# Kernel tuning notes

Measured on AMD Instinct MI355X. Metric: run time of the kernel, lower is better.

The kernel has to match this reference:

```python
import jax, jax.numpy as jnp
import numpy as np

SAMPLE_RATE = 16000
SOUND_SPEED = 343.0
MAX_ORDER = 15
RIR_LENGTH = 3968
WINDOW_LENGTH = 81
PAD = WINDOW_LENGTH // 2  # 40

# Static image-source lattice (depends only on max_order): all integer
# reflection index triplets with |nx|+|ny|+|nz| <= max_order.
_ind = np.arange(-MAX_ORDER, MAX_ORDER + 1)
_grid = np.stack(np.meshgrid(_ind, _ind, _ind, indexing="ij"), -1).reshape(-1, 3)
XYZ = _grid[np.abs(_grid).sum(1) <= MAX_ORDER].astype(np.float32)  # (I,3), I=4991
EXP_LO = np.abs(np.floor(XYZ / 2)).astype(np.float32)        # hits on lower walls per dim
EXP_HI = np.abs(np.floor((XYZ + 1) / 2)).astype(np.float32)  # hits on upper walls per dim


def _hann(x, T):
    # continuous Hann window sampled at non-integer points, zero outside |x|<=T/2
    return jnp.where(jnp.abs(x) <= T / 2, 0.5 * (1.0 + jnp.cos(2.0 * jnp.pi * x / T)), 0.0)


def _forward(inp):
    room = inp[:, 0:3]                 # (B,3) room dimensions [m]
    mic = inp[:, 3:6] * room           # (B,3)
    src = inp[:, 6:9] * room           # (B,3)
    a_w = inp[:, 9:10]
    absorption = jnp.concatenate([a_w, a_w, a_w, a_w, inp[:, 10:11], inp[:, 11:12]], axis=1)
    absorption = absorption * 0.84 + 0.01            # (B,6): [x-,x+,y-,y+,floor,ceiling]
    tr = jnp.sqrt(1.0 - absorption)                  # wall reflection coefficients

    xyz = jnp.asarray(XYZ)                           # (I,3)
    d = room[:, None, :]
    s = src[:, None, :]
    # image source locations (B,I,3): mirror parity per torchaudio ISM
    img_loc = jnp.where(xyz % 2 == 1, d * (xyz + 1.0) - s, d * xyz + s)
    # per-image-source attenuation (B,I)
    t_lo = tr[:, None, 0::2]                         # (B,1,3) lower walls per dim
    t_hi = tr[:, None, 1::2]                         # (B,1,3) upper walls per dim
    att = jnp.prod(t_lo ** jnp.asarray(EXP_LO) * t_hi ** jnp.asarray(EXP_HI), axis=-1)

    dist = jnp.linalg.norm(img_loc - mic[:, None, :], axis=-1)   # (B,I)
    amp = att / dist                                              # 1/r spreading
    delay = dist * (SAMPLE_RATE / SOUND_SPEED)                    # fractional sample delay
    delay_i = jnp.ceil(delay)

    # windowed-sinc fractional-delay pulse sampled at n = delay_i-PAD .. delay_i+PAD
    n_rel = jnp.arange(-PAD, PAD + 1, dtype=jnp.float32)          # (W,)
    x = delay_i[..., None] + n_rel - delay[..., None]             # (B,I,W)
    sig = amp[..., None] * jnp.sinc(x) * _hann(x, 2 * PAD)        # (B,I,W)

    # scatter-accumulate pulses at time index n, dropping out-of-range samples
    t_idx = (delay_i[..., None] + n_rel).astype(jnp.int32)        # (B,I,W)
    B = inp.shape[0]
    b_idx = jnp.arange(B, dtype=jnp.int32)[:, None, None]
    rir = jnp.zeros((B, RIR_LENGTH), dtype=sig.dtype).at[b_idx, t_idx].add(sig, mode="drop")

    toa = PAD + SAMPLE_RATE * jnp.linalg.norm(mic - src, axis=1) / SOUND_SPEED  # (B,)
    return rir, toa


def setup_inputs():
    key = jax.random.key(0)
    u = jax.random.uniform(key, (128, 12), dtype=jnp.float32)
    room = 2.0 + 8.0 * u[:, :3]          # room dims in [2,10] m
    rest = 0.05 + 0.9 * u[:, 3:]         # mic/src fractions and absorptions in (0,1)
    return {"input": jnp.concatenate([room, rest], axis=1)}


def reference(input):
    return _forward(input)
```

## Files before the change

kernel.cpp:

```cpp
#include <hip/hip_runtime.h>

#define NIMG    4991
#define RIRLEN  3968
#define NT      512
#define NW      31
#define KPT     10
#define INV_PI  0.31830988618379067f
#define SR_OVER_C 46.647230320699704f

struct Tab { int v[NIMG]; };
static constexpr Tab make_tab() {
    Tab t{};
    int k = 0;
    for (int x = -15; x <= 15; ++x)
        for (int y = -15; y <= 15; ++y)
            for (int z = -15; z <= 15; ++z) {
                int ax = x < 0 ? -x : x;
                int ay = y < 0 ? -y : y;
                int az = z < 0 ? -z : z;
                if (ax + ay + az <= 15)
                    t.v[k++] = (x + 15) | ((y + 15) << 8) | ((z + 15) << 16);
            }
    return t;
}
__constant__ Tab c_tab = make_tab();

static __device__ __forceinline__ int iabs(int v) { return v < 0 ? -v : v; }

typedef __fp16 f16x2 __attribute__((ext_vector_type(2)));

__global__ __launch_bounds__(NT)
void rir_fused(const float* __restrict__ inp, float* __restrict__ out, int B) {
    const int bx   = blockIdx.x;
    const int b    = bx >> 1;
    const int g    = bx & 1;
    const int tid  = threadIdx.x;
    const int lane = tid & 63;
    const int wv   = tid >> 6;
    const int q    = lane & 3;

    __shared__ float2   s_dh[NIMG];
    __shared__ unsigned s_cs[NIMG];
    __shared__ float    s_par[12];
    __shared__ int      s_h4[256][4];
    __shared__ int      s_off[257];

    for (int k = tid; k < 1024; k += NT) ((int*)s_h4)[k] = 0;
    if (tid == 0) {
        const float* ip = inp + b * 12;
        float rx = ip[0], ry = ip[1], rz = ip[2];
        float mx = ip[3] * rx, my = ip[4] * ry, mz = ip[5] * rz;
        float sx = ip[6] * rx, sy = ip[7] * ry, sz = ip[8] * rz;
        float aw = __builtin_fmaf(ip[9],  0.84f, 0.01f);
        float a4 = __builtin_fmaf(ip[10], 0.84f, 0.01f);
        float a5 = __builtin_fmaf(ip[11], 0.84f, 0.01f);
        s_par[0] = rx; s_par[1] = ry; s_par[2] = rz;
        s_par[3] = mx; s_par[4] = my; s_par[5] = mz;
        s_par[6] = sx; s_par[7] = sy; s_par[8] = sz;
        s_par[9]  = 0.5f * __builtin_amdgcn_logf(1.0f - aw);
        s_par[10] = 0.5f * __builtin_amdgcn_logf(1.0f - a4);
        s_par[11] = 0.5f * __builtin_amdgcn_logf(1.0f - a5);
        if (g == 0) {
            float dx = mx - sx, dy = my - sy, dz = mz - sz;
            out[(size_t)B * RIRLEN + b] = __builtin_fmaf(
                __builtin_sqrtf(dx * dx + dy * dy + dz * dz), SR_OVER_C, 40.0f);
        }
    }
    __syncthreads();

    const float rx = s_par[0], ry = s_par[1], rz = s_par[2];
    const float mx = s_par[3], my = s_par[4], mz = s_par[5];
    const float sx = s_par[6], sy = s_par[7], sz = s_par[8];
    const float lw = s_par[9], l4 = s_par[10], l5 = s_par[11];

    float2   edh[KPT];
    unsigned ecs[KPT];
    int      bkt[KPT];
    #pragma unroll
    for (int k = 0; k < KPT; ++k) {
        bkt[k] = -1;
        const int idx = tid + k * NT;
        if (idx < NIMG) {
            const int p = c_tab.v[idx];
            const int x = (p & 255) - 15;
            const int y = ((p >> 8) & 255) - 15;
            const int z = ((p >> 16) & 255) - 15;
            const float ix = (x & 1) ? __builtin_fmaf(rx, (float)(x + 1), -sx)
                                     : __builtin_fmaf(rx, (float)x, sx);
            const float iy = (y & 1) ? __builtin_fmaf(ry, (float)(y + 1), -sy)
                                     : __builtin_fmaf(ry, (float)y, sy);
            const float iz = (z & 1) ? __builtin_fmaf(rz, (float)(z + 1), -sz)
                                     : __builtin_fmaf(rz, (float)z, sz);
            const float dx = ix - mx, dy = iy - my, dz = iz - mz;
            const float dist  = __builtin_sqrtf(
                __builtin_fmaf(dx, dx, __builtin_fmaf(dy, dy, dz * dz)));
            const float delay = dist * SR_OVER_C;
            const float di    = __builtin_ceilf(delay);
            const int   ti0   = (int)di - 40;
            if (ti0 < RIRLEN) {
                const int ew = iabs(x >> 1) + iabs((x + 1) >> 1)
                             + iabs(y >> 1) + iabs((y + 1) >> 1);
                const float att = __builtin_amdgcn_exp2f(__builtin_fmaf((float)ew, lw,
                                      __builtin_fmaf((float)iabs(z >> 1), l4,
                                           (float)iabs((z + 1) >> 1) * l5)));
                const float amp = att * __builtin_amdgcn_rcpf(dist);
                float frac = di - delay;
                if (frac == 0.0f) frac = di * 1.52587890625e-05f;
                const int dii = (int)di;
                float c1p = amp * __builtin_amdgcn_sinf(0.5f * frac) * INV_PI;
                if (dii & 1) c1p = -c1p;
                const float Hp     = 0.5f * c1p;
                const float dstore = di - frac;
                const float rv = dstore * 0.0125f;
                const float fr = rv - __builtin_floorf(rv);
                const float Hcd = Hp * __builtin_amdgcn_cosf(fr);
                const float Hsd = Hp * __builtin_amdgcn_sinf(fr);
                const f16x2 pk2 = __builtin_amdgcn_cvt_pkrtz(Hcd, Hsd);

                const int bk = (ti0 + 96) >> 4;
                bkt[k] = bk;
                edh[k] = make_float2(dstore, Hp);
                ecs[k] = __builtin_bit_cast(unsigned, pk2);
                atomicAdd(&s_h4[bk][q], 1);
            }
        }
    }
    __syncthreads();

    if (tid < 256)
        s_off[tid + 1] = s_h4[tid][0] + s_h4[tid][1] + s_h4[tid][2] + s_h4[tid][3];
    if (tid == 0) s_off[0] = 0;
    __syncthreads();
    for (int d = 1; d < 256; d <<= 1) {
        int tv = 0;
        if (tid < 256 && tid >= d) tv = s_off[tid + 1 - d];
        __syncthreads();
        if (tid < 256 && tid >= d) s_off[tid + 1] += tv;
        __syncthreads();
    }
    if (tid < 256) {
        int run = s_off[tid];
        #pragma unroll
        for (int p = 0; p < 4; ++p) {
            const int c = s_h4[tid][p];
            s_h4[tid][p] = run;
            run += c;
        }
    }
    __syncthreads();

    #pragma unroll
    for (int k = 0; k < KPT; ++k) {
        if (bkt[k] >= 0) {
            const int slot = atomicAdd(&s_h4[bkt[k]][q], 1);
            s_dh[slot] = edh[k];
            s_cs[slot] = ecs[k];
        }
    }
    __syncthreads();

    int T = 0;
    #pragma unroll
    for (int kk = 0; kk < NW; ++kk) {
        const int wi = g + 2 * kk;
        T += s_off[4 * wi + 10] - s_off[4 * wi + 1];
    }

    int P = 0;
    for (int kk = 0; kk < NW; ++kk) {
        const int wi  = g + 2 * kk;
        const int lo  = s_off[4 * wi + 1];
        const int hi  = s_off[4 * wi + 10];
        const int len = hi - lo;
        int owner = (T > 0)
            ? (int)((8u * (unsigned)(P + (len >> 1))) / (unsigned)T)
            : (kk >> 2);
        if (owner > 7) owner = 7;
        P += len;
        if (owner != wv) continue;

        const int   t    = (wi << 6) + lane;
        const float tf   = (float)t;
        const int   m    = t - (t / 80) * 80;
        const float cth0 = __builtin_amdgcn_cosf((float)m * 0.0125f);
        const float sth0 = __builtin_amdgcn_sinf((float)m * 0.0125f);
        const float sl   = (lane & 1) ? -1.0f : 1.0f;

        float acc = 0.0f;
        #pragma unroll 4
        for (int i = lo; i < hi; ++i) {
            const float2 e  = s_dh[i];
            const f16x2  h  = __builtin_bit_cast(f16x2, s_cs[i]);
            const float xw  = tf - e.x;
            const float pre = __builtin_fmaf(cth0, (float)h.x,
                                  __builtin_fmaf(sth0, (float)h.y, e.y));
            const float hm  = (__builtin_fabsf(xw) <= 40.0f) ? pre : 0.0f;
            acc = __builtin_fmaf(hm, __builtin_amdgcn_rcpf(xw), acc);
        }
        out[(size_t)b * RIRLEN + t] = sl * acc;
    }
}

extern "C" void kernel_launch(void* const* d_in, const int* in_sizes, int n_in,
                              void* d_out, int out_size, void* d_ws, size_t ws_size,
                              hipStream_t stream) {
    (void)d_ws; (void)ws_size; (void)n_in; (void)out_size;
    const float* inp = (const float*)d_in[0];
    float* out = (float*)d_out;
    const int B = in_sizes[0] / 12;
    rir_fused<<<dim3(B * 2), dim3(NT), 0, stream>>>(inp, out, B);
}
```

Before: 105.2 us.

## Split each batch over four blocks and replace block-wide scan with wave scan

Each batch row is now handled by four blocks instead of two. Every block keeps only the image sources whose 16-sample bucket falls inside the windows it owns, so the per-block sort and accumulate work shrinks. The 256-entry prefix scan over bucket counts now runs in a single wavefront using shuffles, replacing the multi-barrier block scan. The trade-off is that each block still recomputes distances for all image sources, the launch has twice as many blocks, and launch bounds now request higher occupancy, which may limit registers.

```diff
diff --git a/kernel.cpp b/kernel.cpp
--- a/kernel.cpp
+++ b/kernel.cpp
@@ -3,7 +3,7 @@
 #define NIMG    4991
 #define RIRLEN  3968
 #define NT      512
-#define NW      31
+#define NGRP    4
 #define KPT     10
 #define INV_PI  0.31830988618379067f
 #define SR_OVER_C 46.647230320699704f
@@ -29,11 +29,11 @@
 
 typedef __fp16 f16x2 __attribute__((ext_vector_type(2)));
 
-__global__ __launch_bounds__(NT)
+__global__ __launch_bounds__(NT, 4)
 void rir_fused(const float* __restrict__ inp, float* __restrict__ out, int B) {
     const int bx   = blockIdx.x;
-    const int b    = bx >> 1;
-    const int g    = bx & 1;
+    const int b    = bx >> 2;
+    const int g    = bx & 3;
     const int tid  = threadIdx.x;
     const int lane = tid & 63;
     const int wv   = tid >> 6;
@@ -72,6 +72,7 @@
     const float mx = s_par[3], my = s_par[4], mz = s_par[5];
     const float sx = s_par[6], sy = s_par[7], sz = s_par[8];
     const float lw = s_par[9], l4 = s_par[10], l5 = s_par[11];
+    const int   fb = 4 * g + 1;
 
     float2   edh[KPT];
     unsigned ecs[KPT];
@@ -97,7 +98,9 @@
             const float delay = dist * SR_OVER_C;
             const float di    = __builtin_ceilf(delay);
             const int   ti0   = (int)di - 40;
-            if (ti0 < RIRLEN) {
+            const int   bk    = (ti0 + 96) >> 4;
+            const bool owned  = ((unsigned)((bk - fb + 16) & 15) < 9u);
+            if (ti0 < RIRLEN && owned) {
                 const int ew = iabs(x >> 1) + iabs((x + 1) >> 1)
                              + iabs(y >> 1) + iabs((y + 1) >> 1);
                 const float att = __builtin_amdgcn_exp2f(__builtin_fmaf((float)ew, lw,
@@ -117,7 +120,6 @@
                 const float Hsd = Hp * __builtin_amdgcn_sinf(fr);
                 const f16x2 pk2 = __builtin_amdgcn_cvt_pkrtz(Hcd, Hsd);
 
-                const int bk = (ti0 + 96) >> 4;
                 bkt[k] = bk;
                 edh[k] = make_float2(dstore, Hp);
                 ecs[k] = __builtin_bit_cast(unsigned, pk2);
@@ -127,17 +129,32 @@
     }
     __syncthreads();
 
-    if (tid < 256)
-        s_off[tid + 1] = s_h4[tid][0] + s_h4[tid][1] + s_h4[tid][2] + s_h4[tid][3];
-    if (tid == 0) s_off[0] = 0;
-    __syncthreads();
-    for (int d = 1; d < 256; d <<= 1) {
-        int tv = 0;
-        if (tid < 256 && tid >= d) tv = s_off[tid + 1 - d];
-        __syncthreads();
-        if (tid < 256 && tid >= d) s_off[tid + 1] += tv;
-        __syncthreads();
-    }
+    if (wv == 0) {
+        const int l = lane;
+        const int4 a0 = *(const int4*)&s_h4[4 * l + 0][0];
+        const int4 a1 = *(const int4*)&s_h4[4 * l + 1][0];
+        const int4 a2 = *(const int4*)&s_h4[4 * l + 2][0];
+        const int4 a3 = *(const int4*)&s_h4[4 * l + 3][0];
+        const int c0 = a0.x + a0.y + a0.z + a0.w;
+        const int c1 = a1.x + a1.y + a1.z + a1.w;
+        const int c2 = a2.x + a2.y + a2.z + a2.w;
+        const int c3 = a3.x + a3.y + a3.z + a3.w;
+        const int ts = c0 + c1 + c2 + c3;
+        int incl = ts;
+        #pragma unroll
+        for (int d = 1; d < 64; d <<= 1) {
+            const int u = __shfl_up(incl, d, 64);
+            if (l >= d) incl += u;
+        }
+        const int base = incl - ts;
+        s_off[4 * l + 0] = base;
+        s_off[4 * l + 1] = base + c0;
+        s_off[4 * l + 2] = base + c0 + c1;
+        s_off[4 * l + 3] = base + c0 + c1 + c2;
+        if (l == 63) s_off[256] = incl;
+    }
+    __syncthreads();
+
     if (tid < 256) {
         int run = s_off[tid];
         #pragma unroll
@@ -161,20 +178,22 @@
 
     int T = 0;
     #pragma unroll
-    for (int kk = 0; kk < NW; ++kk) {
-        const int wi = g + 2 * kk;
-        T += s_off[4 * wi + 10] - s_off[4 * wi + 1];
+    for (int kk = 0; kk < 16; ++kk) {
+        const int wi = g + 4 * kk;
+        if (wi < 62) T += s_off[4 * wi + 10] - s_off[4 * wi + 1];
     }
 
     int P = 0;
-    for (int kk = 0; kk < NW; ++kk) {
-        const int wi  = g + 2 * kk;
+    #pragma unroll
+    for (int kk = 0; kk < 16; ++kk) {
+        const int wi = g + 4 * kk;
+        if (wi >= 62) break;
         const int lo  = s_off[4 * wi + 1];
         const int hi  = s_off[4 * wi + 10];
         const int len = hi - lo;
         int owner = (T > 0)
             ? (int)((8u * (unsigned)(P + (len >> 1))) / (unsigned)T)
-            : (kk >> 2);
+            : (kk >> 1);
         if (owner > 7) owner = 7;
         P += len;
         if (owner != wv) continue;
@@ -208,5 +227,5 @@
     const float* inp = (const float*)d_in[0];
     float* out = (float*)d_out;
     const int B = in_sizes[0] / 12;
-    rir_fused<<<dim3(B * 2), dim3(NT), 0, stream>>>(inp, out, B);
+    rir_fused<<<dim3(B * NGRP), dim3(NT), 0, stream>>>(inp, out, B);
 }
```

Measured after the change: 103.1 us. 1.02x faster.
